# Kernel tuning notes

Hardware: AMD Instinct MI355X
Metric: run time of the kernel (lower is better)

## Reference

```python
import jax, jax.numpy as jnp
import numpy as np

BINS = 10
GHM = 0.75
# edges = [0, 0.1, ..., 1.0], last edge nudged up as in the torch module
_EDGES = np.array([float(i) / BINS for i in range(BINS + 1)], dtype=np.float32)
_EDGES[-1] += 1e-6


def setup_inputs() -> dict:
    key = jax.random.key(0)
    k1, k2 = jax.random.split(key)
    shape = (32, 255, 80, 80)
    pred = jax.random.normal(k1, shape, dtype=jnp.float32)
    target = jax.random.randint(k2, shape, 0, 2).astype(jnp.float32)  # binary labels
    return {"pred": pred, "target": target}


def _ghmc_loss(pred, target):
    target = target.astype(jnp.float32)
    # gradient-norm proxy g = |sigmoid(pred) - target| in [0, 1]
    g = jnp.abs(jax.nn.sigmoid(pred) - target)
    total = float(np.prod(pred.shape))
    weights = jnp.zeros_like(pred)
    # 10-bin histogram weighting; loop over fixed bins is fine (not a data dim).
    # Inclusive edges overlap at boundaries; later bins overwrite, as in torch.
    for i in range(BINS):
        inds = (g >= _EDGES[i]) & (g <= _EDGES[i + 1])
        num_in_bin = jnp.sum(inds)
        # wherever inds is True, num_in_bin >= 1; maximum(.,1) avoids 0-div
        val = GHM * total / jnp.maximum(num_in_bin, 1).astype(pred.dtype)
        weights = jnp.where(inds, val, weights)
    weights = weights / 10.0
    # stable BCE-with-logits: max(x,0) - x*t + log(1 + exp(-|x|))
    bce = jnp.maximum(pred, 0.0) - pred * target + jnp.log1p(jnp.exp(-jnp.abs(pred)))
    return jnp.mean(weights * bce)  # reduction='mean'


def reference(pred, target):
    return _ghmc_loss(pred, target)
```

## Files before the change

kernel.cpp:

```cpp
#include <hip/hip_runtime.h>

#define NBINS 10
#define BLOCK 256
#define NW (BLOCK / 64)

__device__ __forceinline__ void process_elem(float x, float tv,
                                             unsigned int cnt[NBINS],
                                             float fs[NBINS]) {
    const float E[NBINS + 1] = {0.0f, 0.1f, 0.2f, 0.3f, 0.4f, 0.5f,
                                0.6f, 0.7f, 0.8f, 0.9f, 1.000001f};
    float u    = x * (1.0f - 2.0f * tv);
    float au   = fabsf(u);
    float e    = __expf(-au);
    float ope  = 1.0f + e;
    float r    = __builtin_amdgcn_rcpf(ope);
    float g    = (u >= 0.0f) ? r : e * r;
    float bce  = fmaxf(u, 0.0f) + __logf(ope);

    bool ge[NBINS + 1];
    bool gt[NBINS + 1];
    ge[0] = true;  gt[0] = true;
    ge[NBINS] = false; gt[NBINS] = false;
#pragma unroll
    for (int k = 1; k < NBINS; ++k) {
        ge[k] = (g >= E[k]);
        gt[k] = (g >  E[k]);
    }
#pragma unroll
    for (int k = 0; k < NBINS; ++k) {
        cnt[k] += (ge[k] && !gt[k + 1]) ? 1u : 0u;
        fs[k]  += (ge[k] && !ge[k + 1]) ? bce : 0.0f;
    }
}

__global__ __launch_bounds__(BLOCK) void ghmc_main(
    const float* __restrict__ pred, const float* __restrict__ target,
    unsigned int* __restrict__ ws_cnt, float* __restrict__ ws_sum,
    long long nvec, long long ntot, int direct, float* __restrict__ out) {
    unsigned int cnt[NBINS];
    float fs[NBINS];
#pragma unroll
    for (int k = 0; k < NBINS; ++k) { cnt[k] = 0u; fs[k] = 0.0f; }

    const long long stride = (long long)gridDim.x * BLOCK;
    const long long tid0   = (long long)blockIdx.x * BLOCK + threadIdx.x;

    const float4* p4 = (const float4*)pred;
    const float4* t4 = (const float4*)target;
    for (long long i = tid0; i < nvec; i += stride) {
        float4 p = p4[i];
        float4 t = t4[i];
        process_elem(p.x, t.x, cnt, fs);
        process_elem(p.y, t.y, cnt, fs);
        process_elem(p.z, t.z, cnt, fs);
        process_elem(p.w, t.w, cnt, fs);
    }
    {
        long long base = nvec << 2;
        long long rem  = ntot - base;
        if (tid0 < rem) process_elem(pred[base + tid0], target[base + tid0], cnt, fs);
    }

#pragma unroll
    for (int k = 0; k < NBINS; ++k) {
        unsigned int c = cnt[k];
        float        s = fs[k];
#pragma unroll
        for (int off = 32; off > 0; off >>= 1) {
            c += __shfl_down(c, off, 64);
            s += __shfl_down(s, off, 64);
        }
        cnt[k] = c;
        fs[k]  = s;
    }

    __shared__ unsigned int scnt[NW][NBINS];
    __shared__ float        ssum[NW][NBINS];
    int lane = threadIdx.x & 63;
    int wid  = threadIdx.x >> 6;
    if (lane == 0) {
#pragma unroll
        for (int k = 0; k < NBINS; ++k) {
            scnt[wid][k] = cnt[k];
            ssum[wid][k] = fs[k];
        }
    }
    __syncthreads();
    if (threadIdx.x == 0) {
        if (direct) {
            double loss = 0.0;
#pragma unroll
            for (int k = 0; k < NBINS; ++k) {
                unsigned int c = 0;
                double       s = 0.0;
#pragma unroll
                for (int w = 0; w < NW; ++w) { c += scnt[w][k]; s += (double)ssum[w][k]; }
                loss += s / (double)(c > 0u ? c : 1u);
            }
            out[0] = (float)(0.075 * loss);
        } else {
#pragma unroll
            for (int k = 0; k < NBINS; ++k) {
                unsigned int c = 0;
                float        s = 0.0f;
#pragma unroll
                for (int w = 0; w < NW; ++w) { c += scnt[w][k]; s += ssum[w][k]; }
                ws_cnt[(long long)blockIdx.x * NBINS + k] = c;
                ws_sum[(long long)blockIdx.x * NBINS + k] = s;
            }
        }
    }
}

__global__ __launch_bounds__(256) void ghmc_final(
    const unsigned int* __restrict__ ws_cnt, const float* __restrict__ ws_sum,
    int nblocks, float* __restrict__ out) {
    unsigned long long c[NBINS] = {};
    double             s[NBINS] = {};
    for (int b = threadIdx.x; b < nblocks; b += 256) {
#pragma unroll
        for (int k = 0; k < NBINS; ++k) {
            c[k] += ws_cnt[b * NBINS + k];
            s[k] += (double)ws_sum[b * NBINS + k];
        }
    }
#pragma unroll
    for (int k = 0; k < NBINS; ++k) {
        unsigned long long cc = c[k];
        double             ss = s[k];
#pragma unroll
        for (int off = 32; off > 0; off >>= 1) {
            cc += __shfl_down(cc, off, 64);
            ss += __shfl_down(ss, off, 64);
        }
        c[k] = cc;
        s[k] = ss;
    }
    __shared__ unsigned long long sc[4][NBINS];
    __shared__ double             sd[4][NBINS];
    int lane = threadIdx.x & 63;
    int wid  = threadIdx.x >> 6;
    if (lane == 0) {
#pragma unroll
        for (int k = 0; k < NBINS; ++k) { sc[wid][k] = c[k]; sd[wid][k] = s[k]; }
    }
    __syncthreads();
    if (threadIdx.x == 0) {
        double loss = 0.0;
#pragma unroll
        for (int k = 0; k < NBINS; ++k) {
            unsigned long long cc = 0;
            double             ss = 0.0;
#pragma unroll
            for (int w = 0; w < 4; ++w) { cc += sc[w][k]; ss += sd[w][k]; }
            loss += ss / (double)(cc > 0 ? cc : 1ull);
        }
        out[0] = (float)(0.075 * loss);
    }
}

extern "C" void kernel_launch(void* const* d_in, const int* in_sizes, int n_in,
                              void* d_out, int out_size, void* d_ws, size_t ws_size,
                              hipStream_t stream) {
    const float* pred   = (const float*)d_in[0];
    const float* target = (const float*)d_in[1];
    float*       out    = (float*)d_out;
    long long n    = (long long)in_sizes[0];
    long long nvec = n >> 2;

    const size_t per_block = NBINS * (sizeof(unsigned int) + sizeof(float));
    long long g = (nvec + BLOCK - 1) / BLOCK;
    if (g > 2048) g = 2048;
    long long g_ws = (long long)(ws_size / per_block);
    if (g > g_ws) g = g_ws;

    if (g < 1) {
        ghmc_main<<<1, BLOCK, 0, stream>>>(pred, target, nullptr, nullptr,
                                           nvec, n, 1, out);
        return;
    }

    unsigned int* ws_cnt = (unsigned int*)d_ws;
    float*        ws_sum = (float*)((char*)d_ws + (size_t)g * NBINS * sizeof(unsigned int));

    ghmc_main<<<(int)g, BLOCK, 0, stream>>>(pred, target, ws_cnt, ws_sum,
                                            nvec, n, 0, out);
    ghmc_final<<<1, 256, 0, stream>>>(ws_cnt, ws_sum, (int)g, out);
}
```

Baseline: 443.1 us.

## Use cumulative threshold counters and bit-trick sign flip, load 8 elements per iteration

Per-bin counting is replaced by cumulative counts of g>=edge and g>edge, with bin counts recovered by differencing after the loop. This cuts per-element compare and select work. The sign flip is now done with an integer XOR on the target's bit pattern, and log uses log2 scaled by ln2. Each thread loads two float4s per iteration to give more memory-level parallelism. The XOR trick assumes the target is exactly 0.0 or 1.0, and the tail handling for leftovers up to 7 elements only covers tid0 < rem, which is fine only while the grid has enough threads.

```diff
diff --git a/kernel.cpp b/kernel.cpp
--- a/kernel.cpp
+++ b/kernel.cpp
@@ -3,63 +3,80 @@
 #define NBINS 10
 #define BLOCK 256
 #define NW (BLOCK / 64)
+#define GRID_MAX 2048
 
 __device__ __forceinline__ void process_elem(float x, float tv,
-                                             unsigned int cnt[NBINS],
+                                             unsigned G[9], unsigned U[9],
                                              float fs[NBINS]) {
     const float E[NBINS + 1] = {0.0f, 0.1f, 0.2f, 0.3f, 0.4f, 0.5f,
                                 0.6f, 0.7f, 0.8f, 0.9f, 1.000001f};
-    float u    = x * (1.0f - 2.0f * tv);
-    float au   = fabsf(u);
-    float e    = __expf(-au);
-    float ope  = 1.0f + e;
-    float r    = __builtin_amdgcn_rcpf(ope);
-    float g    = (u >= 0.0f) ? r : e * r;
-    float bce  = fmaxf(u, 0.0f) + __logf(ope);
-
-    bool ge[NBINS + 1];
-    bool gt[NBINS + 1];
-    ge[0] = true;  gt[0] = true;
-    ge[NBINS] = false; gt[NBINS] = false;
-#pragma unroll
-    for (int k = 1; k < NBINS; ++k) {
-        ge[k] = (g >= E[k]);
-        gt[k] = (g >  E[k]);
-    }
-#pragma unroll
-    for (int k = 0; k < NBINS; ++k) {
-        cnt[k] += (ge[k] && !gt[k + 1]) ? 1u : 0u;
-        fs[k]  += (ge[k] && !ge[k + 1]) ? bce : 0.0f;
-    }
+    float u   = __uint_as_float(__float_as_uint(x) ^ (__float_as_uint(tv) << 8));
+    float au  = fabsf(u);
+    float e   = __expf(-au);
+    float ope = 1.0f + e;
+    float r   = __builtin_amdgcn_rcpf(ope);
+    float g   = (u >= 0.0f) ? r : e * r;
+    float bce = fmaxf(u, 0.0f) + 0.69314718055994531f * __log2f(ope);
+
+    bool prev = true;
+#pragma unroll
+    for (int k = 1; k <= 9; ++k) {
+        bool ge_k = (g >= E[k]);
+        bool gt_k = (g >  E[k]);
+        G[k - 1] += ge_k ? 1u : 0u;
+        U[k - 1] += gt_k ? 1u : 0u;
+        fs[k - 1] += (prev && !ge_k) ? bce : 0.0f;
+        prev = ge_k;
+    }
+    fs[9] += prev ? bce : 0.0f;
 }
 
 __global__ __launch_bounds__(BLOCK) void ghmc_main(
     const float* __restrict__ pred, const float* __restrict__ target,
     unsigned int* __restrict__ ws_cnt, float* __restrict__ ws_sum,
-    long long nvec, long long ntot, int direct, float* __restrict__ out) {
-    unsigned int cnt[NBINS];
+    long long nvec8, long long ntot, int direct, float* __restrict__ out) {
+    unsigned G[9], U[9];
     float fs[NBINS];
 #pragma unroll
-    for (int k = 0; k < NBINS; ++k) { cnt[k] = 0u; fs[k] = 0.0f; }
+    for (int k = 0; k < 9; ++k) { G[k] = 0u; U[k] = 0u; }
+#pragma unroll
+    for (int k = 0; k < NBINS; ++k) fs[k] = 0.0f;
+    unsigned nloc = 0;
 
     const long long stride = (long long)gridDim.x * BLOCK;
     const long long tid0   = (long long)blockIdx.x * BLOCK + threadIdx.x;
 
     const float4* p4 = (const float4*)pred;
     const float4* t4 = (const float4*)target;
-    for (long long i = tid0; i < nvec; i += stride) {
-        float4 p = p4[i];
-        float4 t = t4[i];
-        process_elem(p.x, t.x, cnt, fs);
-        process_elem(p.y, t.y, cnt, fs);
-        process_elem(p.z, t.z, cnt, fs);
-        process_elem(p.w, t.w, cnt, fs);
+    for (long long i = tid0; i < nvec8; i += stride) {
+        float4 p0 = p4[2 * i];
+        float4 p1 = p4[2 * i + 1];
+        float4 t0 = t4[2 * i];
+        float4 t1 = t4[2 * i + 1];
+        process_elem(p0.x, t0.x, G, U, fs);
+        process_elem(p0.y, t0.y, G, U, fs);
+        process_elem(p0.z, t0.z, G, U, fs);
+        process_elem(p0.w, t0.w, G, U, fs);
+        process_elem(p1.x, t1.x, G, U, fs);
+        process_elem(p1.y, t1.y, G, U, fs);
+        process_elem(p1.z, t1.z, G, U, fs);
+        process_elem(p1.w, t1.w, G, U, fs);
+        nloc += 8;
     }
     {
-        long long base = nvec << 2;
+        long long base = nvec8 << 3;
         long long rem  = ntot - base;
-        if (tid0 < rem) process_elem(pred[base + tid0], target[base + tid0], cnt, fs);
-    }
+        if (tid0 < rem) {
+            process_elem(pred[base + tid0], target[base + tid0], G, U, fs);
+            nloc += 1;
+        }
+    }
+
+    unsigned cnt[NBINS];
+    cnt[0] = nloc - U[0];
+#pragma unroll
+    for (int j = 1; j <= 8; ++j) cnt[j] = G[j - 1] - U[j];
+    cnt[9] = G[8];
 
 #pragma unroll
     for (int k = 0; k < NBINS; ++k) {
@@ -165,18 +182,18 @@
     const float* pred   = (const float*)d_in[0];
     const float* target = (const float*)d_in[1];
     float*       out    = (float*)d_out;
-    long long n    = (long long)in_sizes[0];
-    long long nvec = n >> 2;
+    long long n     = (long long)in_sizes[0];
+    long long nvec8 = n >> 3;
 
     const size_t per_block = NBINS * (sizeof(unsigned int) + sizeof(float));
-    long long g = (nvec + BLOCK - 1) / BLOCK;
-    if (g > 2048) g = 2048;
+    long long g = (nvec8 + BLOCK - 1) / BLOCK;
+    if (g > GRID_MAX) g = GRID_MAX;
     long long g_ws = (long long)(ws_size / per_block);
     if (g > g_ws) g = g_ws;
 
     if (g < 1) {
         ghmc_main<<<1, BLOCK, 0, stream>>>(pred, target, nullptr, nullptr,
-                                           nvec, n, 1, out);
+                                           nvec8, n, 1, out);
         return;
     }
 
@@ -184,6 +201,6 @@
     float*        ws_sum = (float*)((char*)d_ws + (size_t)g * NBINS * sizeof(unsigned int));
 
     ghmc_main<<<(int)g, BLOCK, 0, stream>>>(pred, target, ws_cnt, ws_sum,
-                                            nvec, n, 0, out);
+                                            nvec8, n, 0, out);
     ghmc_final<<<1, 256, 0, stream>>>(ws_cnt, ws_sum, (int)g, out);
 }
```

Result: no change. 444.0 us (+0.2%).
